# Optimization experiments

Hardware: AMD Instinct MI355X
Metric: run time of the kernel (lower is better)

Reference implementation:

```python
import jax, jax.numpy as jnp
import numpy as np

D, H, O, E, K = 512, 2048, 512, 8, 2
CF = 1.0  # capacity_factor


def setup_inputs() -> dict:
    key = jax.random.key(0)
    ks = jax.random.split(key, 4)
    s = lambda k, shape, sc: jax.random.normal(k, shape, jnp.float32) * sc
    return {
        "x": s(ks[0], (8, 2048, D), 1.0),
        "gate_w": s(ks[1], (D, E), D ** -0.5),
        "gate_b": jnp.zeros((E,), jnp.float32),
        "w1": s(ks[2], (E, D, H), D ** -0.5),
        "b1": jnp.zeros((E, H), jnp.float32),
        "w2": s(ks[3], (E, H, O), H ** -0.5),
        "b2": jnp.zeros((E, O), jnp.float32),
    }


def _moe(x, gate_w, gate_b, w1, b1, w2, b2):
    orig = x.shape
    xf = x.reshape(-1, orig[-1])            # [N, D]
    N = xf.shape[0]
    capacity = max(int((N / E) * CF), 4)    # static (shape-derived)

    logits = xf @ gate_w + gate_b           # [N, E]
    gate_probs = jax.nn.softmax(logits, axis=-1)
    topk_p, topk_i = jax.lax.top_k(gate_probs, K)          # [N, K]
    norm_p = topk_p / topk_p.sum(-1, keepdims=True)        # [N, K]

    hot = jax.nn.one_hot(topk_i, E, dtype=xf.dtype)        # [N, K, E]
    mask = hot.sum(1)                                      # [N, E] in {0,1} (top-k indices unique)
    w_te = (norm_p[..., None] * hot).sum(1)                # [N, E] routing weight per token/expert

    def dispatch(m):
        # m: [N] 0/1 mask for one expert; keep first `capacity` tokens in token order
        cs = jnp.cumsum(m)
        keep = (m > 0) & (cs <= capacity)
        idx = jnp.argsort(jnp.where(keep, 0, 1), stable=True)[:capacity]  # kept tokens first, in order
        valid = jnp.arange(capacity) < keep.sum()
        return idx, valid

    idx, valid = jax.vmap(dispatch)(mask.T)                # idx: [E, cap], valid: [E, cap]

    gathered = xf[idx]                                     # [E, cap, D]
    h = jax.nn.gelu(jnp.einsum('ecd,edh->ech', gathered, w1) + b1[:, None, :], approximate=False)
    out = jnp.einsum('ech,eho->eco', h, w2) + b2[:, None, :]  # [E, cap, O]

    wg = w_te[idx, jnp.arange(E)[:, None]]                 # [E, cap] gate weight per dispatched token
    contrib = out * (wg * valid.astype(out.dtype))[..., None]
    combined = jnp.zeros((N, O), out.dtype).at[idx.reshape(-1)].add(contrib.reshape(-1, O))
    return combined.reshape(*orig[:-1], O), gate_probs


def reference(x, gate_w, gate_b, w1, b1, w2, b2):
    return _moe(x, gate_w, gate_b, w1, b1, w2, b2)
```

## Files before the change

kernel.cpp:

```cpp
#include <hip/hip_runtime.h>
#include <hip/hip_bf16.h>

#define NTOK 16384
#define DDIM 512
#define HDIM 2048
#define ODIM 512
#define NE 8
#define CAP 2048

typedef __attribute__((ext_vector_type(8))) short short8v;
typedef __attribute__((ext_vector_type(4))) short short4v;
typedef __attribute__((ext_vector_type(8))) unsigned short ushort8v;
typedef __attribute__((ext_vector_type(4))) float f32x4;

static __device__ __forceinline__ unsigned short f2bf(float f) {
  __hip_bfloat16 h = __float2bfloat16(f);
  return __builtin_bit_cast(unsigned short, h);
}

#define GLOAD_LDS16(gp, lp)                                               \
  __builtin_amdgcn_global_load_lds(                                       \
      (const __attribute__((address_space(1))) void*)(gp),                \
      (__attribute__((address_space(3))) void*)(lp), 16, 0, 0)

__global__ void k_transpose_cvt(const float* __restrict__ src,
                                __hip_bfloat16* __restrict__ dst, int R, int C) {
  __shared__ float tile[32][33];
  int e = blockIdx.z;
  size_t base = (size_t)e * R * C;
  int c0 = blockIdx.x * 32, r0 = blockIdx.y * 32;
  int tx = threadIdx.x, ty = threadIdx.y;
#pragma unroll
  for (int i = 0; i < 32; i += 8)
    tile[ty + i][tx] = src[base + (size_t)(r0 + ty + i) * C + c0 + tx];
  __syncthreads();
#pragma unroll
  for (int i = 0; i < 32; i += 8)
    dst[base + (size_t)(c0 + ty + i) * R + r0 + tx] = __float2bfloat16(tile[tx][ty + i]);
}

__global__ void k_gate(const float* __restrict__ x, const float* __restrict__ gw,
                       const float* __restrict__ gb, float* __restrict__ gate_probs,
                       int2* __restrict__ tk_e, float2* __restrict__ tk_w,
                       int* __restrict__ token_slot) {
  __shared__ float gws[DDIM * 9];
  int tid = threadIdx.x;
  for (int i = tid; i < DDIM * NE; i += 256) {
    int d = i >> 3, e = i & 7;
    gws[d * 9 + e] = gw[i];
  }
  __syncthreads();
  int wid = tid >> 6, lane = tid & 63;
  int t = blockIdx.x * 4 + wid;
  const float* xr = x + (size_t)t * DDIM;
  float acc[NE] = {0.f, 0.f, 0.f, 0.f, 0.f, 0.f, 0.f, 0.f};
#pragma unroll
  for (int j = 0; j < 8; ++j) {
    float xv = xr[lane + 64 * j];
    const float* g = &gws[(lane + 64 * j) * 9];
#pragma unroll
    for (int e = 0; e < NE; ++e) acc[e] += xv * g[e];
  }
#pragma unroll
  for (int e = 0; e < NE; ++e) {
#pragma unroll
    for (int off = 32; off > 0; off >>= 1) acc[e] += __shfl_xor(acc[e], off, 64);
  }
  if (lane == 0) {
    float p[NE];
    float m = -1e30f;
#pragma unroll
    for (int e = 0; e < NE; ++e) { p[e] = acc[e] + gb[e]; m = fmaxf(m, p[e]); }
    float s = 0.f;
#pragma unroll
    for (int e = 0; e < NE; ++e) { p[e] = expf(p[e] - m); s += p[e]; }
    float inv = 1.f / s;
#pragma unroll
    for (int e = 0; e < NE; ++e) { p[e] *= inv; gate_probs[(size_t)t * NE + e] = p[e]; }
    int i1 = 0; float p1 = p[0];
#pragma unroll
    for (int e = 1; e < NE; ++e) if (p[e] > p1) { p1 = p[e]; i1 = e; }
    int i2 = -1; float p2 = -1e30f;
#pragma unroll
    for (int e = 0; e < NE; ++e) if (e != i1 && p[e] > p2) { p2 = p[e]; i2 = e; }
    float wsum = p1 + p2;
    tk_e[t] = make_int2(i1, i2);
    tk_w[t] = make_float2(p1 / wsum, p2 / wsum);
    token_slot[2 * t] = -1;
    token_slot[2 * t + 1] = -1;
  }
}

__global__ void k_dispatch(const int2* __restrict__ tk_e, int* __restrict__ token_slot,
                           int* __restrict__ expert_tokens) {
  int e = blockIdx.x;
  int tid = threadIdx.x;
  int lane = tid & 63, w = tid >> 6;
  __shared__ int wave_cnt[16];
  int base = 0;
  for (int chunk = 0; chunk < NTOK / 1024; ++chunk) {
    int t = chunk * 1024 + tid;
    int2 te = tk_e[t];
    int k = (te.x == e) ? 0 : ((te.y == e) ? 1 : -1);
    bool flag = (k >= 0);
    unsigned long long m = __ballot(flag);
    int pre = __popcll(m & ((1ull << lane) - 1ull));
    __syncthreads();
    if (lane == 0) wave_cnt[w] = __popcll(m);
    __syncthreads();
    int off = 0, total = 0;
#pragma unroll
    for (int i = 0; i < 16; ++i) {
      off += (i < w) ? wave_cnt[i] : 0;
      total += wave_cnt[i];
    }
    int rank = base + off + pre;
    if (flag && rank < CAP) {
      expert_tokens[e * CAP + rank] = t;
      token_slot[2 * t + k] = e * CAP + rank;
    }
    base += total;
  }
  int nvalid = base < CAP ? base : CAP;
  for (int s = nvalid + tid; s < CAP; s += 1024)
    expert_tokens[e * CAP + s] = 0;
}

__global__ void k_gather(const float* __restrict__ x,
                         const int* __restrict__ expert_tokens,
                         __hip_bfloat16* __restrict__ xg) {
  int tid = threadIdx.x, wid = tid >> 6, lane = tid & 63;
  int slot = blockIdx.x * 4 + wid;
  int tok = expert_tokens[slot];
  const float4* src = reinterpret_cast<const float4*>(x + (size_t)tok * DDIM) + lane * 2;
  float4 u = src[0], v = src[1];
  ushort8v o;
  o[0] = f2bf(u.x); o[1] = f2bf(u.y); o[2] = f2bf(u.z); o[3] = f2bf(u.w);
  o[4] = f2bf(v.x); o[5] = f2bf(v.y); o[6] = f2bf(v.z); o[7] = f2bf(v.w);
  *reinterpret_cast<ushort8v*>(xg + (size_t)slot * DDIM + lane * 8) = o;
}

static __device__ __forceinline__ float gelu_fast(float v) {
  float z = 1.5957691216057308f * (v + 0.044715f * v * v * v);
  return v / (1.f + __expf(-z));
}

template <bool GELU, typename OutT>
__global__ __launch_bounds__(256) void k_gemm(
    const __hip_bfloat16* __restrict__ A, const __hip_bfloat16* __restrict__ B,
    const float* __restrict__ bias, OutT* __restrict__ C, int K, int M) {
  __shared__ char lds[3][16384];
  int gx = gridDim.x, gy = gridDim.y;
  int lin = (blockIdx.z * gy + blockIdx.y) * gx + blockIdx.x;
  int total = gx * gy * (int)gridDim.z;
  int cpx = total >> 3;
  lin = (lin & 7) * cpx + (lin >> 3);
  int gxy = gx * gy;
  int e = lin / gxy;
  int rem = lin - e * gxy;
  int mt = rem / gx, nt = rem - mt * gx;

  const int m0 = mt * 128, n0 = nt * 128;
  const int tid = threadIdx.x;
  const int lane = tid & 63, wid = tid >> 6;
  const int wr = wid >> 1, wc = wid & 1;
  const int lrow = lane & 15, kseg = lane >> 4;

  const int r0 = tid >> 2;
  const int sc = (tid & 3) ^ ((r0 >> 1) & 3);
  const int cb0 = (tid & 192) * 16;
  const int cb1 = 4096 + cb0;
  const __hip_bfloat16* Ab = A + ((size_t)e * M + m0) * K;
  const __hip_bfloat16* Bb = B + ((size_t)e * CAP + n0) * K;

#define STAGE(buf, kk)                                                         \
  do {                                                                         \
    GLOAD_LDS16(Ab + (size_t)r0 * K + (kk) + sc * 8, lds[buf] + cb0);          \
    GLOAD_LDS16(Ab + (size_t)(r0 + 64) * K + (kk) + sc * 8, lds[buf] + cb1);   \
    GLOAD_LDS16(Bb + (size_t)r0 * K + (kk) + sc * 8, lds[buf] + 8192 + cb0);   \
    GLOAD_LDS16(Bb + (size_t)(r0 + 64) * K + (kk) + sc * 8, lds[buf] + 8192 + cb1); \
  } while (0)

  f32x4 acc[4][4] = {};
  const int T = K >> 5;
  STAGE(0, 0);
  STAGE(1, 32);
  STAGE(2, 64);
  int cur = 0;
  for (int t = 0; t < T; ++t) {
    if (t < T - 2)       asm volatile("s_waitcnt vmcnt(8)" ::: "memory");
    else if (t == T - 2) asm volatile("s_waitcnt vmcnt(4)" ::: "memory");
    else                 asm volatile("s_waitcnt vmcnt(0)" ::: "memory");
    __builtin_amdgcn_s_barrier();
    const char* AsB = lds[cur];
    const char* BsB = lds[cur] + 8192;
    short8v a[4], b[4];
#pragma unroll
    for (int mm = 0; mm < 4; ++mm) {
      int rr = wr * 64 + mm * 16 + lrow;
      int ks = kseg ^ ((rr >> 1) & 3);
      a[mm] = *reinterpret_cast<const short8v*>(AsB + rr * 64 + ks * 16);
    }
#pragma unroll
    for (int nn = 0; nn < 4; ++nn) {
      int rr = wc * 64 + nn * 16 + lrow;
      int ks = kseg ^ ((rr >> 1) & 3);
      b[nn] = *reinterpret_cast<const short8v*>(BsB + rr * 64 + ks * 16);
    }
    asm volatile("s_waitcnt lgkmcnt(0)" ::: "memory");
    __builtin_amdgcn_sched_barrier(0);
    __builtin_amdgcn_s_barrier();
    if (t + 3 < T) STAGE(cur, (t + 3) << 5);
    __builtin_amdgcn_s_setprio(1);
#pragma unroll
    for (int mm = 0; mm < 4; ++mm)
#pragma unroll
      for (int nn = 0; nn < 4; ++nn)
        acc[mm][nn] = __builtin_amdgcn_mfma_f32_16x16x32_bf16(
            a[mm], b[nn], acc[mm][nn], 0, 0, 0);
    __builtin_amdgcn_s_setprio(0);
    cur = (cur == 2) ? 0 : cur + 1;
  }
#undef STAGE

#pragma unroll
  for (int mm = 0; mm < 4; ++mm) {
    int mrow = m0 + wr * 64 + mm * 16 + kseg * 4;
    float4 bv = *reinterpret_cast<const float4*>(&bias[e * M + mrow]);
#pragma unroll
    for (int nn = 0; nn < 4; ++nn) {
      int token = n0 + wc * 64 + nn * 16 + lrow;
      float v0 = acc[mm][nn][0] + bv.x;
      float v1 = acc[mm][nn][1] + bv.y;
      float v2 = acc[mm][nn][2] + bv.z;
      float v3 = acc[mm][nn][3] + bv.w;
      if (GELU) {
        v0 = gelu_fast(v0); v1 = gelu_fast(v1);
        v2 = gelu_fast(v2); v3 = gelu_fast(v3);
      }
      OutT* cp = C + ((size_t)e * CAP + token) * M + mrow;
      if constexpr (__is_same(OutT, __hip_bfloat16)) {
        short4v o;
        o[0] = (short)f2bf(v0); o[1] = (short)f2bf(v1);
        o[2] = (short)f2bf(v2); o[3] = (short)f2bf(v3);
        *reinterpret_cast<short4v*>(cp) = o;
      } else {
        float4 o = {v0, v1, v2, v3};
        *reinterpret_cast<float4*>(cp) = o;
      }
    }
  }
}

__global__ void k_combine(const float* __restrict__ outbuf,
                          const int* __restrict__ token_slot,
                          const float2* __restrict__ tk_w,
                          float* __restrict__ comb) {
  int tid = threadIdx.x;
  int wid = tid >> 6, lane = tid & 63;
  int t = blockIdx.x * 4 + wid;
  int s0 = token_slot[2 * t], s1 = token_slot[2 * t + 1];
  float2 w = tk_w[t];
  float r[8] = {0.f, 0.f, 0.f, 0.f, 0.f, 0.f, 0.f, 0.f};
  if (s0 >= 0) {
    const float4* p = reinterpret_cast<const float4*>(outbuf + (size_t)s0 * ODIM + lane * 8);
    float4 a = p[0], b = p[1];
    r[0] += w.x * a.x; r[1] += w.x * a.y; r[2] += w.x * a.z; r[3] += w.x * a.w;
    r[4] += w.x * b.x; r[5] += w.x * b.y; r[6] += w.x * b.z; r[7] += w.x * b.w;
  }
  if (s1 >= 0) {
    const float4* p = reinterpret_cast<const float4*>(outbuf + (size_t)s1 * ODIM + lane * 8);
    float4 a = p[0], b = p[1];
    r[0] += w.y * a.x; r[1] += w.y * a.y; r[2] += w.y * a.z; r[3] += w.y * a.w;
    r[4] += w.y * b.x; r[5] += w.y * b.y; r[6] += w.y * b.z; r[7] += w.y * b.w;
  }
  float4* q = reinterpret_cast<float4*>(comb + (size_t)t * ODIM + lane * 8);
  float4 o0 = {r[0], r[1], r[2], r[3]};
  float4 o1 = {r[4], r[5], r[6], r[7]};
  q[0] = o0;
  q[1] = o1;
}

extern "C" void kernel_launch(void* const* d_in, const int* in_sizes, int n_in,
                              void* d_out, int out_size, void* d_ws, size_t ws_size,
                              hipStream_t stream) {
  const float* x      = (const float*)d_in[0];
  const float* gate_w = (const float*)d_in[1];
  const float* gate_b = (const float*)d_in[2];
  const float* w1     = (const float*)d_in[3];
  const float* b1     = (const float*)d_in[4];
  const float* w2     = (const float*)d_in[5];
  const float* b2     = (const float*)d_in[6];

  float* comb = (float*)d_out;
  float* gate_probs = comb + (size_t)NTOK * ODIM;

  char* ws = (char*)d_ws;
  __hip_bfloat16* w1t    = (__hip_bfloat16*)(ws);
  __hip_bfloat16* w2t    = (__hip_bfloat16*)(ws + 16777216);
  __hip_bfloat16* hbuf   = (__hip_bfloat16*)(ws + 33554432);
  __hip_bfloat16* xg     = (__hip_bfloat16*)(ws + 100663296);
  float*          outbuf = (float*)(ws + 100663296);
  int*   expert_tokens   = (int*)(ws + 134217728);
  int2*  tk_e            = (int2*)(ws + 134283264);
  float2* tk_w           = (float2*)(ws + 134414336);
  int*   token_slot      = (int*)(ws + 134545408);

  k_transpose_cvt<<<dim3(HDIM / 32, DDIM / 32, NE), dim3(32, 8), 0, stream>>>(w1, w1t, DDIM, HDIM);
  k_transpose_cvt<<<dim3(ODIM / 32, HDIM / 32, NE), dim3(32, 8), 0, stream>>>(w2, w2t, HDIM, ODIM);
  k_gate<<<NTOK / 4, 256, 0, stream>>>(x, gate_w, gate_b, gate_probs, tk_e, tk_w, token_slot);
  k_dispatch<<<NE, 1024, 0, stream>>>(tk_e, token_slot, expert_tokens);
  k_gather<<<NE * CAP / 4, 256, 0, stream>>>(x, expert_tokens, xg);
  k_gemm<true, __hip_bfloat16>
      <<<dim3(CAP / 128, HDIM / 128, NE), 256, 0, stream>>>(w1t, xg, b1, hbuf, DDIM, HDIM);
  k_gemm<false, float>
      <<<dim3(CAP / 128, ODIM / 128, NE), 256, 0, stream>>>(w2t, hbuf, b2, outbuf, HDIM, ODIM);
  k_combine<<<NTOK / 4, 256, 0, stream>>>(outbuf, token_slot, tk_w, comb);
}
```

Before: 179.7 us.

## Double-buffer LDS fragment registers in GEMM and template K/M dimensions

Restructures the GEMM main loop to unroll by two with ping-pong register fragments. The LDS reads for the next k-step are issued before the MFMAs on the current fragments, removing one barrier per iteration so LDS latency overlaps with matrix math. K and M become compile-time template parameters, and launch bounds request 3 blocks per CU. The extra fragment registers raise register pressure, which could spill or conflict with the occupancy hint.

```diff
diff --git a/kernel.cpp b/kernel.cpp
--- a/kernel.cpp
+++ b/kernel.cpp
@@ -145,10 +145,10 @@
   return v / (1.f + __expf(-z));
 }
 
-template <bool GELU, typename OutT>
-__global__ __launch_bounds__(256) void k_gemm(
+template <int K, int M, bool GELU, typename OutT>
+__global__ __launch_bounds__(256, 3) void k_gemm(
     const __hip_bfloat16* __restrict__ A, const __hip_bfloat16* __restrict__ B,
-    const float* __restrict__ bias, OutT* __restrict__ C, int K, int M) {
+    const float* __restrict__ bias, OutT* __restrict__ C) {
   __shared__ char lds[3][16384];
   int gx = gridDim.x, gy = gridDim.y;
   int lin = (blockIdx.z * gy + blockIdx.y) * gx + blockIdx.x;
@@ -181,47 +181,82 @@
     GLOAD_LDS16(Bb + (size_t)(r0 + 64) * K + (kk) + sc * 8, lds[buf] + 8192 + cb1); \
   } while (0)
 
+#define READF(fa, fb, bi)                                                      \
+  do {                                                                         \
+    const char* AsB_ = lds[bi];                                                \
+    const char* BsB_ = lds[bi] + 8192;                                         \
+    _Pragma("unroll")                                                          \
+    for (int mm = 0; mm < 4; ++mm) {                                           \
+      int rr = wr * 64 + mm * 16 + lrow;                                       \
+      int ks = kseg ^ ((rr >> 1) & 3);                                         \
+      fa[mm] = *reinterpret_cast<const short8v*>(AsB_ + rr * 64 + ks * 16);    \
+    }                                                                          \
+    _Pragma("unroll")                                                          \
+    for (int nn = 0; nn < 4; ++nn) {                                           \
+      int rr = wc * 64 + nn * 16 + lrow;                                       \
+      int ks = kseg ^ ((rr >> 1) & 3);                                         \
+      fb[nn] = *reinterpret_cast<const short8v*>(BsB_ + rr * 64 + ks * 16);    \
+    }                                                                          \
+  } while (0)
+
+#define MFMA16(fa, fb)                                                         \
+  do {                                                                         \
+    __builtin_amdgcn_s_setprio(1);                                             \
+    _Pragma("unroll")                                                          \
+    for (int mm = 0; mm < 4; ++mm)                                             \
+      _Pragma("unroll")                                                        \
+      for (int nn = 0; nn < 4; ++nn)                                           \
+        acc[mm][nn] = __builtin_amdgcn_mfma_f32_16x16x32_bf16(                 \
+            fa[mm], fb[nn], acc[mm][nn], 0, 0, 0);                             \
+    __builtin_amdgcn_s_setprio(0);                                             \
+  } while (0)
+
+#define LGKM0_FENCE()                                                          \
+  do {                                                                         \
+    asm volatile("s_waitcnt lgkmcnt(0)" ::: "memory");                         \
+    __builtin_amdgcn_sched_barrier(0);                                         \
+  } while (0)
+
   f32x4 acc[4][4] = {};
+  short8v pa[4], pb[4], qa[4], qb[4];
   const int T = K >> 5;
+
   STAGE(0, 0);
   STAGE(1, 32);
   STAGE(2, 64);
-  int cur = 0;
-  for (int t = 0; t < T; ++t) {
-    if (t < T - 2)       asm volatile("s_waitcnt vmcnt(8)" ::: "memory");
-    else if (t == T - 2) asm volatile("s_waitcnt vmcnt(4)" ::: "memory");
-    else                 asm volatile("s_waitcnt vmcnt(0)" ::: "memory");
+  asm volatile("s_waitcnt vmcnt(8)" ::: "memory");
+  __builtin_amdgcn_s_barrier();
+  READF(pa, pb, 0);
+  LGKM0_FENCE();
+
+  int bt = 0;
+  for (int t = 0; t < T; t += 2) {
+    int b1 = (bt == 2) ? 0 : bt + 1;
+    int b2 = (b1 == 2) ? 0 : b1 + 1;
+    if (t + 2 < T) asm volatile("s_waitcnt vmcnt(4)" ::: "memory");
+    else           asm volatile("s_waitcnt vmcnt(0)" ::: "memory");
     __builtin_amdgcn_s_barrier();
-    const char* AsB = lds[cur];
-    const char* BsB = lds[cur] + 8192;
-    short8v a[4], b[4];
-#pragma unroll
-    for (int mm = 0; mm < 4; ++mm) {
-      int rr = wr * 64 + mm * 16 + lrow;
-      int ks = kseg ^ ((rr >> 1) & 3);
-      a[mm] = *reinterpret_cast<const short8v*>(AsB + rr * 64 + ks * 16);
+    READF(qa, qb, b1);
+    if (t + 3 < T) STAGE(bt, (t + 3) * 32);
+    __builtin_amdgcn_sched_barrier(0);
+    MFMA16(pa, pb);
+    LGKM0_FENCE();
+    if (t + 2 < T) {
+      if (t + 3 < T) asm volatile("s_waitcnt vmcnt(4)" ::: "memory");
+      else           asm volatile("s_waitcnt vmcnt(0)" ::: "memory");
+      __builtin_amdgcn_s_barrier();
+      READF(pa, pb, b2);
+      if (t + 4 < T) STAGE(b1, (t + 4) * 32);
+      __builtin_amdgcn_sched_barrier(0);
     }
-#pragma unroll
-    for (int nn = 0; nn < 4; ++nn) {
-      int rr = wc * 64 + nn * 16 + lrow;
-      int ks = kseg ^ ((rr >> 1) & 3);
-      b[nn] = *reinterpret_cast<const short8v*>(BsB + rr * 64 + ks * 16);
-    }
-    asm volatile("s_waitcnt lgkmcnt(0)" ::: "memory");
-    __builtin_amdgcn_sched_barrier(0);
-    __builtin_amdgcn_s_barrier();
-    if (t + 3 < T) STAGE(cur, (t + 3) << 5);
-    __builtin_amdgcn_s_setprio(1);
-#pragma unroll
-    for (int mm = 0; mm < 4; ++mm)
-#pragma unroll
-      for (int nn = 0; nn < 4; ++nn)
-        acc[mm][nn] = __builtin_amdgcn_mfma_f32_16x16x32_bf16(
-            a[mm], b[nn], acc[mm][nn], 0, 0, 0);
-    __builtin_amdgcn_s_setprio(0);
-    cur = (cur == 2) ? 0 : cur + 1;
+    MFMA16(qa, qb);
+    LGKM0_FENCE();
+    bt = b2;
   }
 #undef STAGE
+#undef READF
+#undef MFMA16
+#undef LGKM0_FENCE
 
 #pragma unroll
   for (int mm = 0; mm < 4; ++mm) {
@@ -311,9 +346,9 @@
   k_gate<<<NTOK / 4, 256, 0, stream>>>(x, gate_w, gate_b, gate_probs, tk_e, tk_w, token_slot);
   k_dispatch<<<NE, 1024, 0, stream>>>(tk_e, token_slot, expert_tokens);
   k_gather<<<NE * CAP / 4, 256, 0, stream>>>(x, expert_tokens, xg);
-  k_gemm<true, __hip_bfloat16>
-      <<<dim3(CAP / 128, HDIM / 128, NE), 256, 0, stream>>>(w1t, xg, b1, hbuf, DDIM, HDIM);
-  k_gemm<false, float>
-      <<<dim3(CAP / 128, ODIM / 128, NE), 256, 0, stream>>>(w2t, hbuf, b2, outbuf, HDIM, ODIM);
+  k_gemm<DDIM, HDIM, true, __hip_bfloat16>
+      <<<dim3(CAP / 128, HDIM / 128, NE), 256, 0, stream>>>(w1t, xg, b1, hbuf);
+  k_gemm<HDIM, ODIM, false, float>
+      <<<dim3(CAP / 128, ODIM / 128, NE), 256, 0, stream>>>(w2t, hbuf, b2, outbuf);
   k_combine<<<NTOK / 4, 256, 0, stream>>>(outbuf, token_slot, tk_w, comb);
 }
```

New measurement: 174.4 us. -2.9%, faster.

## Enlarge GEMM tile to 256x128, double-buffer LDS, and fuse prep kernels

Applied to the files above, without the earlier changes.

The GEMM tile grows from 128x128 to 256x128 on the weight dimension. Each wave now computes 8x4 MFMA accumulators, with A fragments read in two halves so LDS reads overlap the MFMAs. The LDS pipeline changes from three stages to two, K and M become template constants, and launch bounds ask for two blocks per CU. The two weight transpose kernels and the gate kernel are merged into one launch to cut launch overhead. The larger tile raises register pressure and halves the number of blocks, which can lower occupancy and load balance.

```diff
diff --git a/kernel.cpp b/kernel.cpp
--- a/kernel.cpp
+++ b/kernel.cpp
@@ -23,13 +23,15 @@
       (const __attribute__((address_space(1))) void*)(gp),                \
       (__attribute__((address_space(3))) void*)(lp), 16, 0, 0)
 
-__global__ void k_transpose_cvt(const float* __restrict__ src,
-                                __hip_bfloat16* __restrict__ dst, int R, int C) {
+__device__ __forceinline__ void transpose_block(const float* __restrict__ src,
+                                                __hip_bfloat16* __restrict__ dst,
+                                                int R, int C, int b) {
   __shared__ float tile[32][33];
-  int e = blockIdx.z;
+  int nx = C >> 5, ny = R >> 5;
+  int x = b % nx, y = (b / nx) % ny, e = b / (nx * ny);
   size_t base = (size_t)e * R * C;
-  int c0 = blockIdx.x * 32, r0 = blockIdx.y * 32;
-  int tx = threadIdx.x, ty = threadIdx.y;
+  int c0 = x * 32, r0 = y * 32;
+  int tx = threadIdx.x & 31, ty = threadIdx.x >> 5;
 #pragma unroll
   for (int i = 0; i < 32; i += 8)
     tile[ty + i][tx] = src[base + (size_t)(r0 + ty + i) * C + c0 + tx];
@@ -39,10 +41,16 @@
     dst[base + (size_t)(c0 + ty + i) * R + r0 + tx] = __float2bfloat16(tile[tx][ty + i]);
 }
 
-__global__ void k_gate(const float* __restrict__ x, const float* __restrict__ gw,
-                       const float* __restrict__ gb, float* __restrict__ gate_probs,
+__global__ void k_prep(const float* __restrict__ x, const float* __restrict__ gw,
+                       const float* __restrict__ gb, const float* __restrict__ w1,
+                       __hip_bfloat16* __restrict__ w1t, const float* __restrict__ w2,
+                       __hip_bfloat16* __restrict__ w2t, float* __restrict__ gate_probs,
                        int2* __restrict__ tk_e, float2* __restrict__ tk_w,
                        int* __restrict__ token_slot) {
+  int b = blockIdx.x;
+  if (b < 8192) { transpose_block(w1, w1t, DDIM, HDIM, b); return; }
+  if (b < 16384) { transpose_block(w2, w2t, HDIM, ODIM, b - 8192); return; }
+  b -= 16384;
   __shared__ float gws[DDIM * 9];
   int tid = threadIdx.x;
   for (int i = tid; i < DDIM * NE; i += 256) {
@@ -51,7 +59,7 @@
   }
   __syncthreads();
   int wid = tid >> 6, lane = tid & 63;
-  int t = blockIdx.x * 4 + wid;
+  int t = b * 4 + wid;
   const float* xr = x + (size_t)t * DDIM;
   float acc[NE] = {0.f, 0.f, 0.f, 0.f, 0.f, 0.f, 0.f, 0.f};
 #pragma unroll
@@ -145,11 +153,11 @@
   return v / (1.f + __expf(-z));
 }
 
-template <bool GELU, typename OutT>
-__global__ __launch_bounds__(256) void k_gemm(
+template <int K, int M, bool GELU, typename OutT>
+__global__ __launch_bounds__(256, 2) void k_gemm(
     const __hip_bfloat16* __restrict__ A, const __hip_bfloat16* __restrict__ B,
-    const float* __restrict__ bias, OutT* __restrict__ C, int K, int M) {
-  __shared__ char lds[3][16384];
+    const float* __restrict__ bias, OutT* __restrict__ C) {
+  __shared__ char lds[2][24576];
   int gx = gridDim.x, gy = gridDim.y;
   int lin = (blockIdx.z * gy + blockIdx.y) * gx + blockIdx.x;
   int total = gx * gy * (int)gridDim.z;
@@ -160,7 +168,7 @@
   int rem = lin - e * gxy;
   int mt = rem / gx, nt = rem - mt * gx;
 
-  const int m0 = mt * 128, n0 = nt * 128;
+  const int m0 = mt * 256, n0 = nt * 128;
   const int tid = threadIdx.x;
   const int lane = tid & 63, wid = tid >> 6;
   const int wr = wid >> 1, wc = wid & 1;
@@ -168,85 +176,111 @@
 
   const int r0 = tid >> 2;
   const int sc = (tid & 3) ^ ((r0 >> 1) & 3);
-  const int cb0 = (tid & 192) * 16;
-  const int cb1 = 4096 + cb0;
+  const int cb = (tid & 192) * 16;
   const __hip_bfloat16* Ab = A + ((size_t)e * M + m0) * K;
   const __hip_bfloat16* Bb = B + ((size_t)e * CAP + n0) * K;
 
-#define STAGE(buf, kk)                                                         \
-  do {                                                                         \
-    GLOAD_LDS16(Ab + (size_t)r0 * K + (kk) + sc * 8, lds[buf] + cb0);          \
-    GLOAD_LDS16(Ab + (size_t)(r0 + 64) * K + (kk) + sc * 8, lds[buf] + cb1);   \
-    GLOAD_LDS16(Bb + (size_t)r0 * K + (kk) + sc * 8, lds[buf] + 8192 + cb0);   \
-    GLOAD_LDS16(Bb + (size_t)(r0 + 64) * K + (kk) + sc * 8, lds[buf] + 8192 + cb1); \
+#define STAGE(buf, kk)                                                           \
+  do {                                                                           \
+    _Pragma("unroll")                                                            \
+    for (int j = 0; j < 4; ++j)                                                  \
+      GLOAD_LDS16(Ab + (size_t)(r0 + 64 * j) * K + (kk) + sc * 8,                \
+                  lds[buf] + j * 4096 + cb);                                     \
+    _Pragma("unroll")                                                            \
+    for (int j = 0; j < 2; ++j)                                                  \
+      GLOAD_LDS16(Bb + (size_t)(r0 + 64 * j) * K + (kk) + sc * 8,                \
+                  lds[buf] + 16384 + j * 4096 + cb);                             \
   } while (0)
 
-  f32x4 acc[4][4] = {};
+#define READ_A(dst, bi, half)                                                    \
+  do {                                                                           \
+    _Pragma("unroll")                                                            \
+    for (int mm = 0; mm < 4; ++mm) {                                             \
+      int rr = wr * 128 + (half) * 64 + mm * 16 + lrow;                          \
+      int ks = kseg ^ ((rr >> 1) & 3);                                           \
+      dst[mm] = *reinterpret_cast<const short8v*>(lds[bi] + rr * 64 + ks * 16);  \
+    }                                                                            \
+  } while (0)
+
+#define READ_B(dst, bi)                                                          \
+  do {                                                                           \
+    _Pragma("unroll")                                                            \
+    for (int nn = 0; nn < 4; ++nn) {                                             \
+      int rr = wc * 64 + nn * 16 + lrow;                                         \
+      int ks = kseg ^ ((rr >> 1) & 3);                                           \
+      dst[nn] = *reinterpret_cast<const short8v*>(lds[bi] + 16384 + rr * 64 +    \
+                                                  ks * 16);                      \
+    }                                                                            \
+  } while (0)
+
+#define MFMA_HALF(afr, half)                                                     \
+  do {                                                                           \
+    __builtin_amdgcn_s_setprio(1);                                               \
+    _Pragma("unroll")                                                            \
+    for (int mm = 0; mm < 4; ++mm)                                               \
+      _Pragma("unroll")                                                          \
+      for (int nn = 0; nn < 4; ++nn)                                             \
+        acc[(half) * 4 + mm][nn] = __builtin_amdgcn_mfma_f32_16x16x32_bf16(      \
+            afr[mm], bfr[nn], acc[(half) * 4 + mm][nn], 0, 0, 0);                \
+    __builtin_amdgcn_s_setprio(0);                                               \
+  } while (0)
+
+  f32x4 acc[8][4] = {};
+  short8v a0[4], a1[4], bfr[4];
   const int T = K >> 5;
+
   STAGE(0, 0);
   STAGE(1, 32);
-  STAGE(2, 64);
-  int cur = 0;
+  int bt = 0;
   for (int t = 0; t < T; ++t) {
-    if (t < T - 2)       asm volatile("s_waitcnt vmcnt(8)" ::: "memory");
-    else if (t == T - 2) asm volatile("s_waitcnt vmcnt(4)" ::: "memory");
-    else                 asm volatile("s_waitcnt vmcnt(0)" ::: "memory");
+    if (t < T - 1) asm volatile("s_waitcnt vmcnt(6)" ::: "memory");
+    else           asm volatile("s_waitcnt vmcnt(0)" ::: "memory");
     __builtin_amdgcn_s_barrier();
-    const char* AsB = lds[cur];
-    const char* BsB = lds[cur] + 8192;
-    short8v a[4], b[4];
-#pragma unroll
-    for (int mm = 0; mm < 4; ++mm) {
-      int rr = wr * 64 + mm * 16 + lrow;
-      int ks = kseg ^ ((rr >> 1) & 3);
-      a[mm] = *reinterpret_cast<const short8v*>(AsB + rr * 64 + ks * 16);
-    }
-#pragma unroll
-    for (int nn = 0; nn < 4; ++nn) {
-      int rr = wc * 64 + nn * 16 + lrow;
-      int ks = kseg ^ ((rr >> 1) & 3);
-      b[nn] = *reinterpret_cast<const short8v*>(BsB + rr * 64 + ks * 16);
-    }
+    READ_A(a0, bt, 0);
+    READ_B(bfr, bt);
+    asm volatile("s_waitcnt lgkmcnt(0)" ::: "memory");
+    __builtin_amdgcn_sched_barrier(0);
+    READ_A(a1, bt, 1);
+    MFMA_HALF(a0, 0);
     asm volatile("s_waitcnt lgkmcnt(0)" ::: "memory");
     __builtin_amdgcn_sched_barrier(0);
     __builtin_amdgcn_s_barrier();
-    if (t + 3 < T) STAGE(cur, (t + 3) << 5);
-    __builtin_amdgcn_s_setprio(1);
-#pragma unroll
-    for (int mm = 0; mm < 4; ++mm)
-#pragma unroll
-      for (int nn = 0; nn < 4; ++nn)
-        acc[mm][nn] = __builtin_amdgcn_mfma_f32_16x16x32_bf16(
-            a[mm], b[nn], acc[mm][nn], 0, 0, 0);
-    __builtin_amdgcn_s_setprio(0);
-    cur = (cur == 2) ? 0 : cur + 1;
+    if (t + 2 < T) STAGE(bt, (t + 2) * 32);
+    MFMA_HALF(a1, 1);
+    bt ^= 1;
   }
 #undef STAGE
-
-#pragma unroll
-  for (int mm = 0; mm < 4; ++mm) {
-    int mrow = m0 + wr * 64 + mm * 16 + kseg * 4;
-    float4 bv = *reinterpret_cast<const float4*>(&bias[e * M + mrow]);
-#pragma unroll
-    for (int nn = 0; nn < 4; ++nn) {
-      int token = n0 + wc * 64 + nn * 16 + lrow;
-      float v0 = acc[mm][nn][0] + bv.x;
-      float v1 = acc[mm][nn][1] + bv.y;
-      float v2 = acc[mm][nn][2] + bv.z;
-      float v3 = acc[mm][nn][3] + bv.w;
-      if (GELU) {
-        v0 = gelu_fast(v0); v1 = gelu_fast(v1);
-        v2 = gelu_fast(v2); v3 = gelu_fast(v3);
-      }
-      OutT* cp = C + ((size_t)e * CAP + token) * M + mrow;
-      if constexpr (__is_same(OutT, __hip_bfloat16)) {
-        short4v o;
-        o[0] = (short)f2bf(v0); o[1] = (short)f2bf(v1);
-        o[2] = (short)f2bf(v2); o[3] = (short)f2bf(v3);
-        *reinterpret_cast<short4v*>(cp) = o;
-      } else {
-        float4 o = {v0, v1, v2, v3};
-        *reinterpret_cast<float4*>(cp) = o;
+#undef READ_A
+#undef READ_B
+#undef MFMA_HALF
+
+#pragma unroll
+  for (int half = 0; half < 2; ++half) {
+#pragma unroll
+    for (int mm = 0; mm < 4; ++mm) {
+      int mrow = m0 + wr * 128 + half * 64 + mm * 16 + kseg * 4;
+      float4 bv = *reinterpret_cast<const float4*>(&bias[e * M + mrow]);
+#pragma unroll
+      for (int nn = 0; nn < 4; ++nn) {
+        int token = n0 + wc * 64 + nn * 16 + lrow;
+        float v0 = acc[half * 4 + mm][nn][0] + bv.x;
+        float v1 = acc[half * 4 + mm][nn][1] + bv.y;
+        float v2 = acc[half * 4 + mm][nn][2] + bv.z;
+        float v3 = acc[half * 4 + mm][nn][3] + bv.w;
+        if (GELU) {
+          v0 = gelu_fast(v0); v1 = gelu_fast(v1);
+          v2 = gelu_fast(v2); v3 = gelu_fast(v3);
+        }
+        OutT* cp = C + ((size_t)e * CAP + token) * M + mrow;
+        if constexpr (__is_same(OutT, __hip_bfloat16)) {
+          short4v o;
+          o[0] = (short)f2bf(v0); o[1] = (short)f2bf(v1);
+          o[2] = (short)f2bf(v2); o[3] = (short)f2bf(v3);
+          *reinterpret_cast<short4v*>(cp) = o;
+        } else {
+          float4 o = {v0, v1, v2, v3};
+          *reinterpret_cast<float4*>(cp) = o;
+        }
       }
     }
   }
@@ -306,14 +340,13 @@
   float2* tk_w           = (float2*)(ws + 134414336);
   int*   token_slot      = (int*)(ws + 134545408);
 
-  k_transpose_cvt<<<dim3(HDIM / 32, DDIM / 32, NE), dim3(32, 8), 0, stream>>>(w1, w1t, DDIM, HDIM);
-  k_transpose_cvt<<<dim3(ODIM / 32, HDIM / 32, NE), dim3(32, 8), 0, stream>>>(w2, w2t, HDIM, ODIM);
-  k_gate<<<NTOK / 4, 256, 0, stream>>>(x, gate_w, gate_b, gate_probs, tk_e, tk_w, token_slot);
+  k_prep<<<16384 + NTOK / 4, 256, 0, stream>>>(x, gate_w, gate_b, w1, w1t, w2, w2t,
+                                               gate_probs, tk_e, tk_w, token_slot);
   k_dispatch<<<NE, 1024, 0, stream>>>(tk_e, token_slot, expert_tokens);
   k_gather<<<NE * CAP / 4, 256, 0, stream>>>(x, expert_tokens, xg);
-  k_gemm<true, __hip_bfloat16>
-      <<<dim3(CAP / 128, HDIM / 128, NE), 256, 0, stream>>>(w1t, xg, b1, hbuf, DDIM, HDIM);
-  k_gemm<false, float>
-      <<<dim3(CAP / 128, ODIM / 128, NE), 256, 0, stream>>>(w2t, hbuf, b2, outbuf, HDIM, ODIM);
+  k_gemm<DDIM, HDIM, true, __hip_bfloat16>
+      <<<dim3(CAP / 128, HDIM / 256, NE), 256, 0, stream>>>(w1t, xg, b1, hbuf);
+  k_gemm<HDIM, ODIM, false, float>
+      <<<dim3(CAP / 128, ODIM / 256, NE), 256, 0, stream>>>(w2t, hbuf, b2, outbuf);
   k_combine<<<NTOK / 4, 256, 0, stream>>>(outbuf, token_slot, tk_w, comb);
 }
```

After: 174.5 us. -2.9%, faster.
